# Optimization experiments

Measured on AMD Instinct MI355X. Metric: run time of the kernel, lower is better.

The kernel has to match this reference:

```python
import jax, jax.numpy as jnp
import numpy as np

HIDDEN = 4096
NUM_HEADS = 32
HEAD_DIM = HIDDEN // NUM_HEADS


def _fp8_roundtrip(x):
    # emulate torch float8_e4m3fn weight storage
    return x.astype(jnp.float8_e4m3fn).astype(jnp.float32)


def setup_inputs() -> dict:
    key = jax.random.key(0)
    ks = jax.random.split(key, 10)
    B, S = 2, 4096
    hidden_states = jax.random.normal(ks[0], (B, S, HIDDEN), dtype=jnp.float32)
    scale = 0.02
    def lin(kw, kb):
        w = jax.random.normal(kw, (HIDDEN, HIDDEN), dtype=jnp.float32) * scale
        b = jax.random.normal(kb, (HIDDEN,), dtype=jnp.float32) * scale
        return w, b
    wq, bq = lin(ks[1], ks[2])
    wk, bk = lin(ks[3], ks[4])
    wv, bv = lin(ks[5], ks[6])
    wl, bl = lin(ks[7], ks[8])
    # fp8-quantized Q/K/V projections (latent projection stays fp32)
    wq, bq = _fp8_roundtrip(wq), _fp8_roundtrip(bq)
    wk, bk = _fp8_roundtrip(wk), _fp8_roundtrip(bk)
    wv, bv = _fp8_roundtrip(wv), _fp8_roundtrip(bv)
    return {"hidden_states": hidden_states, "wq": wq, "bq": bq, "wk": wk,
            "bk": bk, "wv": wv, "bv": bv, "wl": wl, "bl": bl}


def reference(hidden_states, wq, bq, wk, bk, wv, bv, wl, bl):
    B, S, E = hidden_states.shape
    H, D = NUM_HEADS, HEAD_DIM
    q = (hidden_states @ wq.T + bq).reshape(B, S, H, D)
    k = (hidden_states @ wk.T + bk).reshape(B, S, H, D)
    v = (hidden_states @ wv.T + bv).reshape(B, S, H, D)
    latent = hidden_states @ wl.T + bl  # computed but unused, as in source
    # NOTE: source does NOT transpose to [B,H,S,D]; scores are [B,S,H,H]
    scores = jnp.einsum('bshd,bstd->bsht', q, k) / np.sqrt(D).astype(np.float32)
    probs = jax.nn.softmax(scores, axis=-1)
    context = jnp.einsum('bsht,bstd->bshd', probs, v).reshape(B, S, E)
    return context
```

## Files before the change

kernel.cpp:

```cpp
#include <hip/hip_runtime.h>
#include <stdint.h>

#define HIDDEN 4096
#define M_TOK 8192
#define KDIM 4096

typedef __attribute__((ext_vector_type(8))) __bf16 bf16x8;
typedef __attribute__((ext_vector_type(4))) float f32x4;
typedef __attribute__((ext_vector_type(8))) unsigned short u16x8;

#define GAS __attribute__((address_space(1)))
#define LAS __attribute__((address_space(3)))

__device__ __forceinline__ unsigned short f2bf(float f) {
  unsigned int u = __float_as_uint(f);
  u += 0x7FFFu + ((u >> 16) & 1u);
  return (unsigned short)(u >> 16);
}
__device__ __forceinline__ float bf2f(unsigned short b) {
  return __uint_as_float(((unsigned int)b) << 16);
}

__device__ __forceinline__ void cvt8(const float* __restrict__ in,
                                     unsigned short* __restrict__ out, int i) {
  const f32x4* p = (const f32x4*)in + (size_t)2 * i;
  f32x4 a = p[0], b = p[1];
  u16x8 o;
  o[0] = f2bf(a.x); o[1] = f2bf(a.y); o[2] = f2bf(a.z); o[3] = f2bf(a.w);
  o[4] = f2bf(b.x); o[5] = f2bf(b.y); o[6] = f2bf(b.z); o[7] = f2bf(b.w);
  ((u16x8*)out)[i] = o;
}

__global__ __launch_bounds__(256) void cvt_fused(
    const float* __restrict__ hs, const float* __restrict__ wq,
    const float* __restrict__ wk, const float* __restrict__ wv,
    const float* __restrict__ bq, const float* __restrict__ bk,
    const float* __restrict__ bv,
    unsigned short* __restrict__ hsb, unsigned short* __restrict__ wb,
    float* __restrict__ bias) {
  int b = blockIdx.x;
  int tid = threadIdx.x;
  if (b < 16384) {
    cvt8(hs, hsb, b * 256 + tid);
  } else if (b < 24576) {
    cvt8(wq, wb, (b - 16384) * 256 + tid);
  } else if (b < 32768) {
    cvt8(wk, wb + 16777216, (b - 24576) * 256 + tid);
  } else if (b < 40960) {
    cvt8(wv, wb + 33554432, (b - 32768) * 256 + tid);
  } else {
    int i = (b - 40960) * 256 + tid;
    float v = (i < 4096) ? bq[i] : (i < 8192) ? bk[i - 4096] : bv[i - 8192];
    bias[i] = v;
  }
}

#define BAR() __builtin_amdgcn_s_barrier()
#define PRIO(p) __builtin_amdgcn_s_setprio(p)
#define VMC6() asm volatile("s_waitcnt vmcnt(6)" ::: "memory")
#define VMC4() asm volatile("s_waitcnt vmcnt(4)" ::: "memory")
#define VMC0() asm volatile("s_waitcnt vmcnt(0)" ::: "memory")
#define LGKM(n) do { asm volatile("s_waitcnt lgkmcnt(" #n ")" ::: "memory"); \
  __builtin_amdgcn_sched_barrier(0); } while (0)
#define SB0() __builtin_amdgcn_sched_barrier(0)

__global__ __launch_bounds__(512, 2) void gemm_qkv(
    const unsigned short* __restrict__ A,
    const unsigned short* __restrict__ W,
    const float* __restrict__ bias,
    unsigned short* __restrict__ out) {
  __shared__ __attribute__((aligned(16))) unsigned short lds[65536];

  int tid = threadIdx.x;
  int lane = tid & 63;
  int w = tid >> 6;
  int wm = w >> 2;
  int wn = w & 3;
  int l16 = lane & 15;
  int lk = lane >> 4;

  int bid = blockIdx.x;
  int xcd = bid & 7;
  int local = bid >> 3;
  int r = local >> 5;
  int i = local & 31;
  int tm = (xcd << 2) + (i >> 3);
  int tn = (r << 3) + (i & 7);
  int m0 = tm << 8, n0 = tn << 8;

  int rp = tid >> 3;
  int ce = ((tid & 7) << 3) ^ ((rp & 7) << 3);
  const unsigned short* aSrc = A + (size_t)(m0 + rp) * KDIM + ce;
  const unsigned short* bSrc = W + (size_t)(n0 + rp) * KDIM + ce;
  int tid8 = tid * 8;

#define STA(b, h, kt) do { \
  __builtin_amdgcn_global_load_lds((GAS void*)(aSrc + (size_t)((h)*128) * KDIM + (kt)*64), \
      (LAS void*)(lds + (b)*16384 + (h)*8192 + tid8), 16, 0, 0); \
  __builtin_amdgcn_global_load_lds((GAS void*)(aSrc + (size_t)((h)*128 + 64) * KDIM + (kt)*64), \
      (LAS void*)(lds + (b)*16384 + (h)*8192 + 4096 + tid8), 16, 0, 0); } while (0)
#define STB(b, h, kt) do { \
  __builtin_amdgcn_global_load_lds((GAS void*)(bSrc + (size_t)((h)*128) * KDIM + (kt)*64), \
      (LAS void*)(lds + 32768 + (b)*16384 + (h)*8192 + tid8), 16, 0, 0); \
  __builtin_amdgcn_global_load_lds((GAS void*)(bSrc + (size_t)((h)*128 + 64) * KDIM + (kt)*64), \
      (LAS void*)(lds + 32768 + (b)*16384 + (h)*8192 + 4096 + tid8), 16, 0, 0); } while (0)

  int colbase = (lk << 3) ^ ((l16 & 7) << 3);
  int aRd = wm * 8192 + l16 * 64 + colbase;
  int bRd = (wn >> 1) * 8192 + (wn & 1) * 4096 + l16 * 64 + colbase;

#define RD_A(c, mi, ks) (*(const bf16x8*)(lds + (c)*16384 + (((aRd) + (mi)*1024) ^ ((ks)*32))))
#define RD_B(c, nj, ks) (*(const bf16x8*)(lds + 32768 + (c)*16384 + (((bRd) + (nj)*1024) ^ ((ks)*32))))

  bf16x8 av[8][2];
  bf16x8 bv[4][2];
  f32x4 acc[8][4] = {};

#define RP1(c) do { \
  bv[0][0]=RD_B(c,0,0); bv[0][1]=RD_B(c,0,1); bv[1][0]=RD_B(c,1,0); bv[1][1]=RD_B(c,1,1); \
  bv[2][0]=RD_B(c,2,0); bv[2][1]=RD_B(c,2,1); bv[3][0]=RD_B(c,3,0); bv[3][1]=RD_B(c,3,1); \
  av[0][0]=RD_A(c,0,0); av[0][1]=RD_A(c,0,1); av[1][0]=RD_A(c,1,0); av[1][1]=RD_A(c,1,1); } while (0)
#define RP2(c) do { \
  av[2][0]=RD_A(c,2,0); av[2][1]=RD_A(c,2,1); av[3][0]=RD_A(c,3,0); av[3][1]=RD_A(c,3,1); \
  av[4][0]=RD_A(c,4,0); av[4][1]=RD_A(c,4,1); av[5][0]=RD_A(c,5,0); av[5][1]=RD_A(c,5,1); } while (0)
#define RP3(c) do { \
  av[6][0]=RD_A(c,6,0); av[6][1]=RD_A(c,6,1); av[7][0]=RD_A(c,7,0); av[7][1]=RD_A(c,7,1); } while (0)

#define MFMA2(mi, nj) do { \
  acc[mi][nj] = __builtin_amdgcn_mfma_f32_16x16x32_bf16(av[mi][0], bv[nj][0], acc[mi][nj], 0, 0, 0); \
  acc[mi][nj] = __builtin_amdgcn_mfma_f32_16x16x32_bf16(av[mi][1], bv[nj][1], acc[mi][nj], 0, 0, 0); } while (0)
#define MM(mi) do { MFMA2(mi,0); MFMA2(mi,1); MFMA2(mi,2); MFMA2(mi,3); } while (0)

#define KTILE(c, ka, kb) do { \
  RP1(c); RP2(c); STA(!(c), 1, ka); \
  BAR(); LGKM(8); PRIO(1); MM(0); MM(1); PRIO(0); BAR(); \
  RP3(c); STB(c, 0, kb); \
  BAR(); LGKM(4); PRIO(1); MM(2); MM(3); PRIO(0); BAR(); \
  STB(c, 1, kb); \
  BAR(); LGKM(0); PRIO(1); MM(4); MM(5); PRIO(0); BAR(); \
  STA(c, 0, kb); \
  BAR(); SB0(); PRIO(1); MM(6); MM(7); PRIO(0); VMC6(); BAR(); } while (0)

  STB(0, 0, 0); STB(0, 1, 0); STA(0, 0, 0); STA(0, 1, 0);
  VMC4();
  STB(1, 0, 1); STB(1, 1, 1); STA(1, 0, 1);
  VMC6();
  BAR();

  for (int it = 0; it < 31; ++it) {
    int k1 = 2 * it + 1, k2 = 2 * it + 2, k3 = 2 * it + 3;
    KTILE(0, k1, k2);
    KTILE(1, k2, k3);
  }
  RP1(0); RP2(0); STA(1, 1, 63);
  BAR(); LGKM(8); PRIO(1); MM(0); MM(1); PRIO(0); BAR();
  RP3(0);
  BAR(); LGKM(4); PRIO(1); MM(2); MM(3); PRIO(0); BAR();
  BAR(); LGKM(0); PRIO(1); MM(4); MM(5); PRIO(0); BAR();
  BAR(); SB0(); PRIO(1); MM(6); MM(7); PRIO(0); VMC0(); BAR();
  RP1(1); RP2(1);
  BAR(); LGKM(8); PRIO(1); MM(0); MM(1); PRIO(0); BAR();
  RP3(1);
  BAR(); LGKM(4); PRIO(1); MM(2); MM(3); PRIO(0); BAR();
  BAR(); LGKM(0); PRIO(1); MM(4); MM(5); PRIO(0); BAR();
  BAR(); SB0(); PRIO(1); MM(6); MM(7); PRIO(0);

  int matc = n0 >> 12;
  int ncol = (n0 & 4095) + wn * 64;
  unsigned short* O = out + (size_t)matc * M_TOK * HIDDEN;
  float bb[4];
#pragma unroll
  for (int nj = 0; nj < 4; ++nj) bb[nj] = bias[n0 + wn * 64 + nj * 16 + l16];
#pragma unroll
  for (int mi = 0; mi < 8; ++mi) {
#pragma unroll
    for (int rr = 0; rr < 4; ++rr) {
      int row = m0 + wm * 128 + mi * 16 + lk * 4 + rr;
      size_t rb = (size_t)row * HIDDEN + ncol + l16;
#pragma unroll
      for (int nj = 0; nj < 4; ++nj)
        O[rb + nj * 16] = f2bf(acc[mi][nj][rr] + bb[nj]);
    }
  }
}

__global__ __launch_bounds__(256) void attn_kernel(const unsigned short* __restrict__ qkv,
                                                   float* __restrict__ out) {
  __shared__ float sQ[32 * 132];
  __shared__ float sK[32 * 132];
  __shared__ float sV[32 * 132];
  __shared__ float sP[32 * 33];

  int m = blockIdx.x;
  int tid = threadIdx.x;
  const unsigned short* gq = qkv + (size_t)m * HIDDEN;
  const unsigned short* gk = gq + (size_t)M_TOK * HIDDEN;
  const unsigned short* gv = gk + (size_t)M_TOK * HIDDEN;

  int row = tid >> 3;
  int cb = (tid & 7) << 4;
  int go = row * 128 + cb;
  int lo = row * 132 + cb;
  {
    u16x8 x0 = *(const u16x8*)(gq + go);
    u16x8 x1 = *(const u16x8*)(gq + go + 8);
#pragma unroll
    for (int j = 0; j < 8; ++j) { sQ[lo + j] = bf2f(x0[j]); sQ[lo + 8 + j] = bf2f(x1[j]); }
    x0 = *(const u16x8*)(gk + go);
    x1 = *(const u16x8*)(gk + go + 8);
#pragma unroll
    for (int j = 0; j < 8; ++j) { sK[lo + j] = bf2f(x0[j]); sK[lo + 8 + j] = bf2f(x1[j]); }
    x0 = *(const u16x8*)(gv + go);
    x1 = *(const u16x8*)(gv + go + 8);
#pragma unroll
    for (int j = 0; j < 8; ++j) { sV[lo + j] = bf2f(x0[j]); sV[lo + 8 + j] = bf2f(x1[j]); }
  }
  __syncthreads();

  int h = tid >> 3;
  int t4 = (tid & 7) << 2;
  const f32x4* qr = (const f32x4*)(sQ + h * 132);
  const f32x4* k0 = (const f32x4*)(sK + (t4 + 0) * 132);
  const f32x4* k1 = (const f32x4*)(sK + (t4 + 1) * 132);
  const f32x4* k2 = (const f32x4*)(sK + (t4 + 2) * 132);
  const f32x4* k3 = (const f32x4*)(sK + (t4 + 3) * 132);
  float s0 = 0.f, s1 = 0.f, s2 = 0.f, s3 = 0.f;
#pragma unroll
  for (int d = 0; d < 32; ++d) {
    f32x4 q = qr[d];
    f32x4 a = k0[d]; s0 += q.x * a.x + q.y * a.y + q.z * a.z + q.w * a.w;
    f32x4 b = k1[d]; s1 += q.x * b.x + q.y * b.y + q.z * b.z + q.w * b.w;
    f32x4 c = k2[d]; s2 += q.x * c.x + q.y * c.y + q.z * c.z + q.w * c.w;
    f32x4 e = k3[d]; s3 += q.x * e.x + q.y * e.y + q.z * e.z + q.w * e.w;
  }
  const float scale = 0.08838834764831845f;
  s0 *= scale; s1 *= scale; s2 *= scale; s3 *= scale;
  float mx = fmaxf(fmaxf(s0, s1), fmaxf(s2, s3));
  mx = fmaxf(mx, __shfl_xor(mx, 1));
  mx = fmaxf(mx, __shfl_xor(mx, 2));
  mx = fmaxf(mx, __shfl_xor(mx, 4));
  float e0 = __expf(s0 - mx), e1 = __expf(s1 - mx), e2 = __expf(s2 - mx), e3 = __expf(s3 - mx);
  float sum = e0 + e1 + e2 + e3;
  sum += __shfl_xor(sum, 1);
  sum += __shfl_xor(sum, 2);
  sum += __shfl_xor(sum, 4);
  float inv = 1.0f / sum;
  sP[h * 33 + t4 + 0] = e0 * inv;
  sP[h * 33 + t4 + 1] = e1 * inv;
  sP[h * 33 + t4 + 2] = e2 * inv;
  sP[h * 33 + t4 + 3] = e3 * inv;
  __syncthreads();

  int d0 = (tid & 7) << 4;
  f32x4 o0 = {0.f, 0.f, 0.f, 0.f}, o1 = o0, o2 = o0, o3 = o0;
  const float* pr = sP + h * 33;
#pragma unroll
  for (int t = 0; t < 32; ++t) {
    float p = pr[t];
    const f32x4* vr = (const f32x4*)(sV + t * 132 + d0);
    o0 += p * vr[0];
    o1 += p * vr[1];
    o2 += p * vr[2];
    o3 += p * vr[3];
  }
  f32x4* op = (f32x4*)(out + (size_t)m * HIDDEN + h * 128 + d0);
  op[0] = o0; op[1] = o1; op[2] = o2; op[3] = o3;
}

extern "C" void kernel_launch(void* const* d_in, const int* in_sizes, int n_in,
                              void* d_out, int out_size, void* d_ws, size_t ws_size,
                              hipStream_t stream) {
  const float* hs = (const float*)d_in[0];
  const float* wq = (const float*)d_in[1];
  const float* bq = (const float*)d_in[2];
  const float* wk = (const float*)d_in[3];
  const float* bk = (const float*)d_in[4];
  const float* wv = (const float*)d_in[5];
  const float* bv = (const float*)d_in[6];

  char* ws = (char*)d_ws;
  const size_t HS_OFF = 0;
  const size_t W_OFF = 67108864;
  const size_t QKV_OFF = 167772160;
  const size_t BIAS_OFF = 369098752;
  const size_t NEED = 369147904;
  if (ws_size < NEED) return;

  unsigned short* hsb = (unsigned short*)(ws + HS_OFF);
  unsigned short* wb = (unsigned short*)(ws + W_OFF);
  unsigned short* qkv = (unsigned short*)(ws + QKV_OFF);
  float* bias = (float*)(ws + BIAS_OFF);

  cvt_fused<<<41008, 256, 0, stream>>>(hs, wq, wk, wv, bq, bk, bv, hsb, wb, bias);
  gemm_qkv<<<1536, 512, 0, stream>>>(hsb, wb, bias, qkv);
  attn_kernel<<<8192, 256, 0, stream>>>(qkv, (float*)d_out);
}
```

Measured before the change: 865.0 us.

## Software-pipeline LDS fragment reads one phase ahead of MFMA groups

Restructures the GEMM K-loop so each phase's LDS register reads for the next A/B fragments are issued right after that phase's MFMAs, with a full lgkmcnt(0) wait at the start of the next phase. The aim is to overlap LDS read latency with matrix compute instead of waiting on partial lgkmcnt counts before each MFMA group. Prologue and epilogue are rewritten to match, and the prologue now waits for all loads (vmcnt 0). This risks LDS hazards if next-tile reads overlap buffers still being written, and adds register pressure from fragments being live across phases.

```diff
diff --git a/kernel.cpp b/kernel.cpp
--- a/kernel.cpp
+++ b/kernel.cpp
@@ -58,9 +58,8 @@
 #define BAR() __builtin_amdgcn_s_barrier()
 #define PRIO(p) __builtin_amdgcn_s_setprio(p)
 #define VMC6() asm volatile("s_waitcnt vmcnt(6)" ::: "memory")
-#define VMC4() asm volatile("s_waitcnt vmcnt(4)" ::: "memory")
 #define VMC0() asm volatile("s_waitcnt vmcnt(0)" ::: "memory")
-#define LGKM(n) do { asm volatile("s_waitcnt lgkmcnt(" #n ")" ::: "memory"); \
+#define LGKM0() do { asm volatile("s_waitcnt lgkmcnt(0)" ::: "memory"); \
   __builtin_amdgcn_sched_barrier(0); } while (0)
 #define SB0() __builtin_amdgcn_sched_barrier(0)
 
@@ -132,38 +131,36 @@
 #define MM(mi) do { MFMA2(mi,0); MFMA2(mi,1); MFMA2(mi,2); MFMA2(mi,3); } while (0)
 
 #define KTILE(c, ka, kb) do { \
-  RP1(c); RP2(c); STA(!(c), 1, ka); \
-  BAR(); LGKM(8); PRIO(1); MM(0); MM(1); PRIO(0); BAR(); \
-  RP3(c); STB(c, 0, kb); \
-  BAR(); LGKM(4); PRIO(1); MM(2); MM(3); PRIO(0); BAR(); \
+  STA(!(c), 1, ka); \
+  BAR(); LGKM0(); PRIO(1); MM(0); MM(1); RP2(c); PRIO(0); SB0(); BAR(); \
+  STB(c, 0, kb); \
+  BAR(); LGKM0(); PRIO(1); MM(2); MM(3); RP3(c); PRIO(0); SB0(); BAR(); \
   STB(c, 1, kb); \
-  BAR(); LGKM(0); PRIO(1); MM(4); MM(5); PRIO(0); BAR(); \
-  STA(c, 0, kb); \
-  BAR(); SB0(); PRIO(1); MM(6); MM(7); PRIO(0); VMC6(); BAR(); } while (0)
+  BAR(); LGKM0(); PRIO(1); MM(4); MM(5); PRIO(0); SB0(); BAR(); \
+  STA(c, 0, kb); VMC6(); \
+  BAR(); SB0(); PRIO(1); MM(6); MM(7); RP1(!(c)); PRIO(0); SB0(); BAR(); } while (0)
 
   STB(0, 0, 0); STB(0, 1, 0); STA(0, 0, 0); STA(0, 1, 0);
-  VMC4();
   STB(1, 0, 1); STB(1, 1, 1); STA(1, 0, 1);
-  VMC6();
+  VMC0();
   BAR();
+  RP1(0);
 
   for (int it = 0; it < 31; ++it) {
     int k1 = 2 * it + 1, k2 = 2 * it + 2, k3 = 2 * it + 3;
     KTILE(0, k1, k2);
     KTILE(1, k2, k3);
   }
-  RP1(0); RP2(0); STA(1, 1, 63);
-  BAR(); LGKM(8); PRIO(1); MM(0); MM(1); PRIO(0); BAR();
-  RP3(0);
-  BAR(); LGKM(4); PRIO(1); MM(2); MM(3); PRIO(0); BAR();
-  BAR(); LGKM(0); PRIO(1); MM(4); MM(5); PRIO(0); BAR();
-  BAR(); SB0(); PRIO(1); MM(6); MM(7); PRIO(0); VMC0(); BAR();
-  RP1(1); RP2(1);
-  BAR(); LGKM(8); PRIO(1); MM(0); MM(1); PRIO(0); BAR();
-  RP3(1);
-  BAR(); LGKM(4); PRIO(1); MM(2); MM(3); PRIO(0); BAR();
-  BAR(); LGKM(0); PRIO(1); MM(4); MM(5); PRIO(0); BAR();
-  BAR(); SB0(); PRIO(1); MM(6); MM(7); PRIO(0);
+  STA(1, 1, 63);
+  BAR(); LGKM0(); PRIO(1); MM(0); MM(1); RP2(0); PRIO(0); SB0(); BAR();
+  BAR(); LGKM0(); PRIO(1); MM(2); MM(3); RP3(0); PRIO(0); SB0(); BAR();
+  BAR(); LGKM0(); PRIO(1); MM(4); MM(5); PRIO(0); SB0(); BAR();
+  VMC0();
+  BAR(); SB0(); PRIO(1); MM(6); MM(7); RP1(1); PRIO(0); SB0(); BAR();
+  BAR(); LGKM0(); PRIO(1); MM(0); MM(1); RP2(1); PRIO(0); SB0(); BAR();
+  BAR(); LGKM0(); PRIO(1); MM(2); MM(3); RP3(1); PRIO(0); SB0(); BAR();
+  BAR(); LGKM0(); PRIO(1); MM(4); MM(5); PRIO(0); SB0(); BAR();
+  BAR(); LGKM0(); PRIO(1); MM(6); MM(7); PRIO(0);
 
   int matc = n0 >> 12;
   int ncol = (n0 & 4095) + wn * 64;
```

Measured after the change: 838.2 us. 3.1% less time.
